# Performance work log

Hardware: AMD Instinct MI355X
Metric: run time of the kernel (lower is better)

The kernel has to match this reference:

```python
import jax, jax.numpy as jnp
import numpy as np


def setup_inputs() -> dict:
    key = jax.random.key(0)
    k1, k2, k3 = jax.random.split(key, 3)
    B, N, D = 16, 4096, 64
    q = jax.random.normal(k1, (B, N, D), dtype=jnp.float32)
    k = jax.random.normal(k2, (B, N, D), dtype=jnp.float32)
    v = jax.random.normal(k3, (B, N, D), dtype=jnp.float32)
    return {"q": q, "k": k, "v": v}


def reference(q, k, v):
    # attention = softmax(q @ k^T, axis=2)  (scale=None in the torch module,
    # dropout=0.0 is identity)
    scores = jnp.einsum("bnd,bmd->bnm", q, k)          # [B, N, N]
    attention = jax.nn.softmax(scores, axis=2)          # softmax over keys
    context = jnp.einsum("bnm,bmd->bnd", attention, v)  # [B, N, D]
    return (context, attention)
```

## Files before the change

### kernel.cpp

```cpp
#include <hip/hip_runtime.h>
#include <hip/hip_bf16.h>

typedef _Float16 half8 __attribute__((ext_vector_type(8)));
typedef _Float16 half4 __attribute__((ext_vector_type(4)));
typedef short short8 __attribute__((ext_vector_type(8)));
typedef short short4v __attribute__((ext_vector_type(4)));
typedef float f32x4 __attribute__((ext_vector_type(4)));

#define BATCH 16
#define SEQ   4096
#define DIM   64
#define MTILE 64
#define KVB   64
#define NCH   (SEQ / KVB)
#define EL_CH 4096
#define EL_B  (NCH * EL_CH)

__device__ __forceinline__ short f2bf(float f) {
    unsigned u = __builtin_bit_cast(unsigned, f);
    u += 0x7FFF + ((u >> 16) & 1);
    return (short)(u >> 16);
}
__device__ __forceinline__ float bf2f(short h) {
    return __builtin_bit_cast(float, (unsigned)((unsigned short)h) << 16);
}

__device__ __forceinline__ void gld16(const void* g, void* l) {
    __builtin_amdgcn_global_load_lds(
        (const __attribute__((address_space(1))) unsigned int*)g,
        (__attribute__((address_space(3))) unsigned int*)l, 16, 0, 0);
}

__global__ __launch_bounds__(256) void preconvert(
    const float* __restrict__ k, const float* __restrict__ v,
    _Float16* __restrict__ kh, _Float16* __restrict__ vh)
{
    int f = blockIdx.x * 256 + threadIdx.x;
    int lane = f & 63;
    int sub  = (f >> 6) & 7;
    int ch   = (f >> 9) & 63;
    int bb   = (f >> 15) & 15;
    int isV  = f >> 19;
    int nf = sub >> 1, kk = sub & 1;
    size_t fo = (size_t)(f & ((1 << 19) - 1)) * 8;

    if (!isV) {
        int key = ch * 64 + nf * 16 + (lane & 15);
        int d0  = kk * 32 + (lane >> 4) * 8;
        const float* src = k + (((size_t)bb * SEQ + key) * DIM + d0);
        half8 h8;
        #pragma unroll
        for (int e = 0; e < 8; ++e) h8[e] = (_Float16)src[e];
        *(half8*)(kh + fo) = h8;
    } else {
        int kr0 = kk * 32 + (lane >> 4) * 8;
        int d   = nf * 16 + (lane & 15);
        const float* src = v + (((size_t)bb * SEQ + ch * 64 + kr0) * DIM + d);
        half8 h8;
        #pragma unroll
        for (int e = 0; e < 8; ++e) h8[e] = (_Float16)src[e * DIM];
        *(half8*)(vh + fo) = h8;
    }
}

__global__ __launch_bounds__(256) void attn_main(
    const float* __restrict__ q, const _Float16* __restrict__ kh,
    const _Float16* __restrict__ vh, float* __restrict__ ctx,
    float* __restrict__ att)
{
    __shared__ _Float16 Kst[2][EL_CH];
    __shared__ _Float16 Vst[2][EL_CH];
    __shared__ _Float16 Ph[4][16][72];

    int id = blockIdx.x;
    int bb = (id & 7) + 8 * (id >> 9);
    int qt = (id >> 3) & 63;

    int tid = threadIdx.x;
    int w = tid >> 6, lane = tid & 63, li = lane & 15, h4 = lane >> 4;

    int qrow = qt * MTILE + w * 16 + li;
    const float* qp = q + ((size_t)bb * SEQ + qrow) * DIM;
    half8 aq[2];
    #pragma unroll
    for (int kk = 0; kk < 2; ++kk)
        #pragma unroll
        for (int e = 0; e < 8; ++e)
            aq[kk][e] = (_Float16)qp[kk * 32 + h4 * 8 + e];

    const _Float16* khb = kh + (size_t)bb * EL_B;
    const _Float16* vvb = vh + (size_t)bb * EL_B;

    auto stage_k = [&](int buf, int ch) {
        const _Float16* g = khb + (size_t)ch * EL_CH + tid * 8;
        gld16(g,        &Kst[buf][w * 512]);
        gld16(g + 2048, &Kst[buf][2048 + w * 512]);
    };
    auto stage_v = [&](int buf, int ch) {
        const _Float16* g = vvb + (size_t)ch * EL_CH + tid * 8;
        gld16(g,        &Vst[buf][w * 512]);
        gld16(g + 2048, &Vst[buf][2048 + w * 512]);
    };
    auto qkt = [&](int buf, f32x4* s) {
        const half8* k8 = (const half8*)&Kst[buf][0];
        #pragma unroll
        for (int kk = 0; kk < 2; ++kk)
            #pragma unroll
            for (int nf = 0; nf < 4; ++nf)
                s[nf] = __builtin_amdgcn_mfma_f32_16x16x32_f16(
                    k8[(nf * 2 + kk) * 64 + lane], aq[kk], s[nf], 0, 0, 0);
    };

    float ll = 0.f;

    stage_k(0, 0);
    for (int ch = 0; ch < NCH; ++ch) {
        int buf = ch & 1;
        if (ch + 1 < NCH) {
            stage_k(buf ^ 1, ch + 1);
            asm volatile("s_waitcnt vmcnt(2)" ::: "memory");
        } else {
            asm volatile("s_waitcnt vmcnt(0)" ::: "memory");
        }
        __builtin_amdgcn_s_barrier();
        asm volatile("" ::: "memory");

        f32x4 s[4];
        #pragma unroll
        for (int nf = 0; nf < 4; ++nf) s[nf] = (f32x4){0.f, 0.f, 0.f, 0.f};
        qkt(buf, s);

        float a = 0.f;
        #pragma unroll
        for (int nf = 0; nf < 4; ++nf)
            #pragma unroll
            for (int r = 0; r < 4; ++r)
                a += __expf(s[nf][r]);
        ll += a;

        asm volatile("" ::: "memory");
        __builtin_amdgcn_s_barrier();
    }

    ll += __shfl_xor(ll, 16);
    ll += __shfl_xor(ll, 32);
    float rl = 1.0f / ll;

    f32x4 acc[4];
    #pragma unroll
    for (int nf = 0; nf < 4; ++nf) acc[nf] = (f32x4){0.f, 0.f, 0.f, 0.f};

    float* attb = att + ((size_t)bb * SEQ + (size_t)qt * MTILE + w * 16) * SEQ;

    stage_k(0, 0); stage_v(0, 0);
    for (int ch = 0; ch < NCH; ++ch) {
        int buf = ch & 1;
        if (ch + 1 < NCH) {
            stage_k(buf ^ 1, ch + 1);
            stage_v(buf ^ 1, ch + 1);
            if (ch == 0) asm volatile("s_waitcnt vmcnt(4)" ::: "memory");
            else         asm volatile("s_waitcnt vmcnt(8)" ::: "memory");
        } else {
            asm volatile("s_waitcnt vmcnt(4)" ::: "memory");
        }
        __builtin_amdgcn_s_barrier();
        asm volatile("" ::: "memory");

        f32x4 s[4];
        #pragma unroll
        for (int nf = 0; nf < 4; ++nf) s[nf] = (f32x4){0.f, 0.f, 0.f, 0.f};
        qkt(buf, s);

        #pragma unroll
        for (int nf = 0; nf < 4; ++nf) {
            half4 p4;
            #pragma unroll
            for (int r = 0; r < 4; ++r)
                p4[r] = (_Float16)(__expf(s[nf][r]) * rl);
            *(half4*)&Ph[w][li][nf * 16 + h4 * 4] = p4;
        }

        #pragma unroll
        for (int j = 0; j < 4; ++j) {
            int row = j * 4 + h4;
            half4 ph = *(const half4*)&Ph[w][row][li * 4];
            f32x4 pv = { (float)ph[0], (float)ph[1], (float)ph[2], (float)ph[3] };
            __builtin_nontemporal_store(
                pv, (f32x4*)(attb + (size_t)row * SEQ + ch * KVB + li * 4));
        }

        const half8* v8 = (const half8*)&Vst[buf][0];
        #pragma unroll
        for (int kk = 0; kk < 2; ++kk) {
            half8 pa = *(const half8*)&Ph[w][li][kk * 32 + h4 * 8];
            #pragma unroll
            for (int nf = 0; nf < 4; ++nf)
                acc[nf] = __builtin_amdgcn_mfma_f32_16x16x32_f16(
                    pa, v8[(nf * 2 + kk) * 64 + lane], acc[nf], 0, 0, 0);
        }

        asm volatile("" ::: "memory");
        __builtin_amdgcn_s_barrier();
    }

    float* ctxb = ctx + ((size_t)bb * SEQ + (size_t)qt * MTILE + w * 16) * DIM;
    #pragma unroll
    for (int nf = 0; nf < 4; ++nf)
        #pragma unroll
        for (int r = 0; r < 4; ++r)
            __builtin_nontemporal_store(
                acc[nf][r], &ctxb[(size_t)(4 * h4 + r) * DIM + nf * 16 + li]);
}

__global__ __launch_bounds__(256) void attn_fallback(
    const float* __restrict__ q, const float* __restrict__ k,
    const float* __restrict__ v, float* __restrict__ ctx,
    float* __restrict__ att)
{
    __shared__ short K_hi[KVB][72];
    __shared__ short K_lo[KVB][72];
    __shared__ short V_lds[DIM][72];
    __shared__ short P_lds[4][16][72];

    int id = blockIdx.x;
    int bb = (id & 7) + 8 * (id >> 9);
    int qt = (id >> 3) & 63;
    int tid = threadIdx.x;
    int w = tid >> 6, lane = tid & 63, li = lane & 15, h4 = lane >> 4;

    int qrow = qt * 64 + w * 16 + li;
    const float* qp = q + ((size_t)bb * SEQ + qrow) * DIM;
    short8 aq[2], aql[2];
    #pragma unroll
    for (int kk = 0; kk < 2; ++kk)
        #pragma unroll
        for (int e = 0; e < 8; ++e) {
            float x = qp[kk * 32 + h4 * 8 + e];
            short h = f2bf(x);
            aq[kk][e] = h; aql[kk][e] = f2bf(x - bf2f(h));
        }

    float m[4], l[4];
    #pragma unroll
    for (int r = 0; r < 4; ++r) { m[r] = -3.0e38f; l[r] = 0.0f; }
    const float* kbase = k + (size_t)bb * SEQ * DIM;
    const float* vbase = v + (size_t)bb * SEQ * DIM;

    for (int ch = 0; ch < NCH; ++ch) {
        __syncthreads();
        const float4* kc = (const float4*)(kbase + (size_t)ch * KVB * DIM);
        #pragma unroll
        for (int j = 0; j < 4; ++j) {
            int f4 = j * 256 + tid; int key = f4 >> 4, d4 = f4 & 15;
            float4 val = kc[f4];
            short4v h4v, l4v;
            h4v[0]=f2bf(val.x); l4v[0]=f2bf(val.x-bf2f(h4v[0]));
            h4v[1]=f2bf(val.y); l4v[1]=f2bf(val.y-bf2f(h4v[1]));
            h4v[2]=f2bf(val.z); l4v[2]=f2bf(val.z-bf2f(h4v[2]));
            h4v[3]=f2bf(val.w); l4v[3]=f2bf(val.w-bf2f(h4v[3]));
            *(short4v*)&K_hi[key][d4*4] = h4v;
            *(short4v*)&K_lo[key][d4*4] = l4v;
        }
        __syncthreads();
        f32x4 s[4];
        #pragma unroll
        for (int nf = 0; nf < 4; ++nf) s[nf] = (f32x4){0.f,0.f,0.f,0.f};
        #pragma unroll
        for (int kk = 0; kk < 2; ++kk)
            #pragma unroll
            for (int nf = 0; nf < 4; ++nf) {
                short8 kbv = *(const short8*)&K_hi[nf*16+li][kk*32+h4*8];
                short8 klv = *(const short8*)&K_lo[nf*16+li][kk*32+h4*8];
                s[nf] = __builtin_amdgcn_mfma_f32_16x16x32_bf16(aq[kk],  kbv, s[nf],0,0,0);
                s[nf] = __builtin_amdgcn_mfma_f32_16x16x32_bf16(aq[kk],  klv, s[nf],0,0,0);
                s[nf] = __builtin_amdgcn_mfma_f32_16x16x32_bf16(aql[kk], kbv, s[nf],0,0,0);
            }
        #pragma unroll
        for (int r = 0; r < 4; ++r) {
            float cmax = fmaxf(fmaxf(s[0][r],s[1][r]), fmaxf(s[2][r],s[3][r]));
            #pragma unroll
            for (int off = 1; off < 16; off <<= 1) cmax = fmaxf(cmax, __shfl_xor(cmax, off));
            float mnew = fmaxf(m[r], cmax);
            float cs = __expf(s[0][r]-mnew)+__expf(s[1][r]-mnew)+__expf(s[2][r]-mnew)+__expf(s[3][r]-mnew);
            #pragma unroll
            for (int off = 1; off < 16; off <<= 1) cs += __shfl_xor(cs, off);
            l[r] = l[r]*__expf(m[r]-mnew) + cs; m[r] = mnew;
        }
    }
    float rl[4];
    #pragma unroll
    for (int r = 0; r < 4; ++r) rl[r] = 1.0f / l[r];

    f32x4 acc[4];
    #pragma unroll
    for (int nf = 0; nf < 4; ++nf) acc[nf] = (f32x4){0.f,0.f,0.f,0.f};
    float* attb = att + ((size_t)bb * SEQ + (size_t)qt * 64 + w * 16) * SEQ;

    for (int ch = 0; ch < NCH; ++ch) {
        __syncthreads();
        const float4* kc = (const float4*)(kbase + (size_t)ch * KVB * DIM);
        #pragma unroll
        for (int j = 0; j < 4; ++j) {
            int f4 = j * 256 + tid; int key = f4 >> 4, d4 = f4 & 15;
            float4 val = kc[f4];
            short4v h4v, l4v;
            h4v[0]=f2bf(val.x); l4v[0]=f2bf(val.x-bf2f(h4v[0]));
            h4v[1]=f2bf(val.y); l4v[1]=f2bf(val.y-bf2f(h4v[1]));
            h4v[2]=f2bf(val.z); l4v[2]=f2bf(val.z-bf2f(h4v[2]));
            h4v[3]=f2bf(val.w); l4v[3]=f2bf(val.w-bf2f(h4v[3]));
            *(short4v*)&K_hi[key][d4*4] = h4v;
            *(short4v*)&K_lo[key][d4*4] = l4v;
        }
        {
            int key = tid & 63, dblk = (tid >> 6) * 16;
            const float* vc = vbase + ((size_t)ch * KVB + key) * DIM + dblk;
            #pragma unroll
            for (int j = 0; j < 4; ++j) {
                float4 val = *(const float4*)(vc + j * 4);
                V_lds[dblk+j*4+0][key]=f2bf(val.x); V_lds[dblk+j*4+1][key]=f2bf(val.y);
                V_lds[dblk+j*4+2][key]=f2bf(val.z); V_lds[dblk+j*4+3][key]=f2bf(val.w);
            }
        }
        __syncthreads();
        f32x4 s[4];
        #pragma unroll
        for (int nf = 0; nf < 4; ++nf) s[nf] = (f32x4){0.f,0.f,0.f,0.f};
        #pragma unroll
        for (int kk = 0; kk < 2; ++kk)
            #pragma unroll
            for (int nf = 0; nf < 4; ++nf) {
                short8 kbv = *(const short8*)&K_hi[nf*16+li][kk*32+h4*8];
                short8 klv = *(const short8*)&K_lo[nf*16+li][kk*32+h4*8];
                s[nf] = __builtin_amdgcn_mfma_f32_16x16x32_bf16(aq[kk],  kbv, s[nf],0,0,0);
                s[nf] = __builtin_amdgcn_mfma_f32_16x16x32_bf16(aq[kk],  klv, s[nf],0,0,0);
                s[nf] = __builtin_amdgcn_mfma_f32_16x16x32_bf16(aql[kk], kbv, s[nf],0,0,0);
            }
        #pragma unroll
        for (int nf = 0; nf < 4; ++nf)
            #pragma unroll
            for (int r = 0; r < 4; ++r) {
                float p = __expf(s[nf][r] - m[r]) * rl[r];
                __builtin_nontemporal_store(p, &attb[(size_t)(4*h4+r)*SEQ + ch*KVB + nf*16 + li]);
                P_lds[w][4*h4+r][nf*16+li] = f2bf(p);
            }
        #pragma unroll
        for (int kk = 0; kk < 2; ++kk) {
            short8 pa = *(const short8*)&P_lds[w][li][kk*32+h4*8];
            #pragma unroll
            for (int nf = 0; nf < 4; ++nf) {
                short8 vbv = *(const short8*)&V_lds[nf*16+li][kk*32+h4*8];
                acc[nf] = __builtin_amdgcn_mfma_f32_16x16x32_bf16(pa, vbv, acc[nf],0,0,0);
            }
        }
    }
    float* ctxb = ctx + ((size_t)bb * SEQ + (size_t)qt * 64 + w * 16) * DIM;
    #pragma unroll
    for (int nf = 0; nf < 4; ++nf)
        #pragma unroll
        for (int r = 0; r < 4; ++r)
            __builtin_nontemporal_store(acc[nf][r], &ctxb[(size_t)(4*h4+r)*DIM + nf*16 + li]);
}

extern "C" void kernel_launch(void* const* d_in, const int* in_sizes, int n_in,
                              void* d_out, int out_size, void* d_ws, size_t ws_size,
                              hipStream_t stream) {
    const float* q = (const float*)d_in[0];
    const float* k = (const float*)d_in[1];
    const float* v = (const float*)d_in[2];
    float* ctx = (float*)d_out;
    float* att = (float*)d_out + (size_t)BATCH * SEQ * DIM;

    const size_t t_el = (size_t)BATCH * EL_B;
    const size_t need = 2 * t_el * 2;

    if (ws_size >= need) {
        _Float16* kh = (_Float16*)d_ws;
        _Float16* vh = kh + t_el;
        preconvert<<<4096, 256, 0, stream>>>(k, v, kh, vh);
        attn_main<<<BATCH * (SEQ / MTILE), 256, 0, stream>>>(q, kh, vh, ctx, att);
    } else {
        attn_fallback<<<BATCH * (SEQ / 64), 256, 0, stream>>>(q, k, v, ctx, att);
    }
}
```

Before: 304.9 us.

## Stage two K chunks per barrier in pass one and store attention directly from registers

The first (row-sum) pass now loads two 64-key K chunks into a merged LDS buffer per iteration, which halves the number of barriers and waits and doubles the bytes in flight. Shared memory is unified into a single KV array that both passes reuse. In the second pass the attention probabilities are written straight from registers in fp32 instead of taking a round trip through LDS as fp16. This drops the extra LDS reads and the fp16 rounding of the stored output, but each lane now writes 16-byte pieces scattered across rows, which is less contiguous than before.

Measured after the change: 382.9 us. +25.6%, slower.

```diff
diff --git a/kernel.cpp b/kernel.cpp
--- a/kernel.cpp
+++ b/kernel.cpp
@@ -13,6 +13,7 @@
 #define MTILE 64
 #define KVB   64
 #define NCH   (SEQ / KVB)
+#define NSC   (NCH / 2)
 #define EL_CH 4096
 #define EL_B  (NCH * EL_CH)
 
@@ -68,8 +69,7 @@
     const _Float16* __restrict__ vh, float* __restrict__ ctx,
     float* __restrict__ att)
 {
-    __shared__ _Float16 Kst[2][EL_CH];
-    __shared__ _Float16 Vst[2][EL_CH];
+    __shared__ _Float16 KV[2][8192];
     __shared__ _Float16 Ph[4][16][72];
 
     int id = blockIdx.x;
@@ -91,18 +91,8 @@
     const _Float16* khb = kh + (size_t)bb * EL_B;
     const _Float16* vvb = vh + (size_t)bb * EL_B;
 
-    auto stage_k = [&](int buf, int ch) {
-        const _Float16* g = khb + (size_t)ch * EL_CH + tid * 8;
-        gld16(g,        &Kst[buf][w * 512]);
-        gld16(g + 2048, &Kst[buf][2048 + w * 512]);
-    };
-    auto stage_v = [&](int buf, int ch) {
-        const _Float16* g = vvb + (size_t)ch * EL_CH + tid * 8;
-        gld16(g,        &Vst[buf][w * 512]);
-        gld16(g + 2048, &Vst[buf][2048 + w * 512]);
-    };
-    auto qkt = [&](int buf, f32x4* s) {
-        const half8* k8 = (const half8*)&Kst[buf][0];
+    auto qkt = [&](const _Float16* base, f32x4* s) {
+        const half8* k8 = (const half8*)base;
         #pragma unroll
         for (int kk = 0; kk < 2; ++kk)
             #pragma unroll
@@ -113,30 +103,40 @@
 
     float ll = 0.f;
 
-    stage_k(0, 0);
-    for (int ch = 0; ch < NCH; ++ch) {
-        int buf = ch & 1;
-        if (ch + 1 < NCH) {
-            stage_k(buf ^ 1, ch + 1);
-            asm volatile("s_waitcnt vmcnt(2)" ::: "memory");
+    auto stage_sc = [&](int buf, int sc) {
+        const _Float16* g = khb + (size_t)sc * (2 * EL_CH) + tid * 8;
+        gld16(g,        &KV[buf][w * 512]);
+        gld16(g + 2048, &KV[buf][2048 + w * 512]);
+        gld16(g + 4096, &KV[buf][4096 + w * 512]);
+        gld16(g + 6144, &KV[buf][6144 + w * 512]);
+    };
+
+    stage_sc(0, 0);
+    for (int sc = 0; sc < NSC; ++sc) {
+        int buf = sc & 1;
+        if (sc + 1 < NSC) {
+            stage_sc(buf ^ 1, sc + 1);
+            asm volatile("s_waitcnt vmcnt(4)" ::: "memory");
         } else {
             asm volatile("s_waitcnt vmcnt(0)" ::: "memory");
         }
         __builtin_amdgcn_s_barrier();
         asm volatile("" ::: "memory");
 
-        f32x4 s[4];
-        #pragma unroll
-        for (int nf = 0; nf < 4; ++nf) s[nf] = (f32x4){0.f, 0.f, 0.f, 0.f};
-        qkt(buf, s);
-
-        float a = 0.f;
-        #pragma unroll
-        for (int nf = 0; nf < 4; ++nf)
-            #pragma unroll
-            for (int r = 0; r < 4; ++r)
-                a += __expf(s[nf][r]);
-        ll += a;
+        #pragma unroll
+        for (int c2 = 0; c2 < 2; ++c2) {
+            f32x4 s[4];
+            #pragma unroll
+            for (int nf = 0; nf < 4; ++nf) s[nf] = (f32x4){0.f, 0.f, 0.f, 0.f};
+            qkt(&KV[buf][c2 * EL_CH], s);
+            float a = 0.f;
+            #pragma unroll
+            for (int nf = 0; nf < 4; ++nf)
+                #pragma unroll
+                for (int r = 0; r < 4; ++r)
+                    a += __expf(s[nf][r]);
+            ll += a;
+        }
 
         asm volatile("" ::: "memory");
         __builtin_amdgcn_s_barrier();
@@ -150,7 +150,18 @@
     #pragma unroll
     for (int nf = 0; nf < 4; ++nf) acc[nf] = (f32x4){0.f, 0.f, 0.f, 0.f};
 
-    float* attb = att + ((size_t)bb * SEQ + (size_t)qt * MTILE + w * 16) * SEQ;
+    float* attr = att + ((size_t)bb * SEQ + (size_t)qt * MTILE + w * 16 + li) * SEQ;
+
+    auto stage_k = [&](int buf, int ch) {
+        const _Float16* g = khb + (size_t)ch * EL_CH + tid * 8;
+        gld16(g,        &KV[0][buf * EL_CH + w * 512]);
+        gld16(g + 2048, &KV[0][buf * EL_CH + 2048 + w * 512]);
+    };
+    auto stage_v = [&](int buf, int ch) {
+        const _Float16* g = vvb + (size_t)ch * EL_CH + tid * 8;
+        gld16(g,        &KV[1][buf * EL_CH + w * 512]);
+        gld16(g + 2048, &KV[1][buf * EL_CH + 2048 + w * 512]);
+    };
 
     stage_k(0, 0); stage_v(0, 0);
     for (int ch = 0; ch < NCH; ++ch) {
@@ -169,27 +180,24 @@
         f32x4 s[4];
         #pragma unroll
         for (int nf = 0; nf < 4; ++nf) s[nf] = (f32x4){0.f, 0.f, 0.f, 0.f};
-        qkt(buf, s);
+        qkt(&KV[0][buf * EL_CH], s);
 
         #pragma unroll
         for (int nf = 0; nf < 4; ++nf) {
             half4 p4;
-            #pragma unroll
-            for (int r = 0; r < 4; ++r)
-                p4[r] = (_Float16)(__expf(s[nf][r]) * rl);
+            f32x4 pv;
+            #pragma unroll
+            for (int r = 0; r < 4; ++r) {
+                float p = __expf(s[nf][r]) * rl;
+                p4[r] = (_Float16)p;
+                pv[r] = p;
+            }
             *(half4*)&Ph[w][li][nf * 16 + h4 * 4] = p4;
-        }
-
-        #pragma unroll
-        for (int j = 0; j < 4; ++j) {
-            int row = j * 4 + h4;
-            half4 ph = *(const half4*)&Ph[w][row][li * 4];
-            f32x4 pv = { (float)ph[0], (float)ph[1], (float)ph[2], (float)ph[3] };
             __builtin_nontemporal_store(
-                pv, (f32x4*)(attb + (size_t)row * SEQ + ch * KVB + li * 4));
-        }
-
-        const half8* v8 = (const half8*)&Vst[buf][0];
+                pv, (f32x4*)(attr + ch * KVB + nf * 16 + h4 * 4));
+        }
+
+        const half8* v8 = (const half8*)&KV[1][buf * EL_CH];
         #pragma unroll
         for (int kk = 0; kk < 2; ++kk) {
             half8 pa = *(const half8*)&Ph[w][li][kk * 32 + h4 * 8];
```
